# Kernel tuning notes

Hardware: AMD Instinct MI355X
Metric: run time of the kernel (lower is better)

The kernel has to match this reference:

```python
import jax, jax.numpy as jnp
import numpy as np
from jax.ops import segment_sum, segment_max

N, E, DS, DZ = 16384, 262144, 384, 128
H, D, PQ, PV = 12, 16, 4, 8
EPS = 1e-8


def _quat_to_rot(q):
    q = q / jnp.linalg.norm(q, axis=-1, keepdims=True)
    w, x, y, z = q[:, 0], q[:, 1], q[:, 2], q[:, 3]
    R = jnp.stack([
        1 - 2 * (y * y + z * z), 2 * (x * y - w * z), 2 * (x * z + w * y),
        2 * (x * y + w * z), 1 - 2 * (x * x + z * z), 2 * (y * z - w * x),
        2 * (x * z - w * y), 2 * (y * z + w * x), 1 - 2 * (x * x + y * y),
    ], axis=-1).reshape(-1, 3, 3)
    return R


def setup_inputs() -> dict:
    key = jax.random.key(0)
    ks = jax.random.split(key, 20)
    s = jax.random.normal(ks[0], (N, DS), jnp.float32)
    z = jax.random.normal(ks[1], (E, DZ), jnp.float32)
    edge_index = jax.random.randint(ks[2], (E, 2), 0, N, jnp.int64)
    # valid rigid frames: rotation from random unit quaternion + translation
    R = _quat_to_rot(jax.random.normal(ks[3], (N, 4), jnp.float32))
    t = jax.random.normal(ks[4], (N, 3), jnp.float32)
    f = jnp.zeros((N, 4, 4), jnp.float32).at[:, :3, :3].set(R)
    f = f.at[:, :3, 3].set(t).at[:, 3, 3].set(1.0)

    def lin(k, dout, din):
        return jax.random.normal(k, (dout, din), jnp.float32) / np.sqrt(din)

    hc, hpqk, hpv = H * D, H * PQ * 3, H * PV * 3
    s_out_dim = H * (D * 2 + PV * 4)
    params = dict(
        Wq=lin(ks[5], hc, DS), bq=jnp.zeros((hc,), jnp.float32),
        Wk=lin(ks[6], hc, DS), bk=jnp.zeros((hc,), jnp.float32),
        Wv=lin(ks[7], hc, DS), bv=jnp.zeros((hc,), jnp.float32),
        Wb=lin(ks[8], H, DZ), bb=jnp.zeros((H,), jnp.float32),
        Wqp=lin(ks[9], hpqk, DS), bqp=jnp.zeros((hpqk,), jnp.float32),
        Wkp=lin(ks[10], hpqk, DS), bkp=jnp.zeros((hpqk,), jnp.float32),
        Wvp=lin(ks[11], hpv, DS), bvp=jnp.zeros((hpv,), jnp.float32),
        head_weights=jnp.full((H,), 0.541324854612918, jnp.float32),
        Wpair=lin(ks[12], hc, DZ), bpair=jnp.zeros((hc,), jnp.float32),
        Wo=lin(ks[13], DS, s_out_dim), bo=jnp.zeros((DS,), jnp.float32),
    )
    return dict(s=s, z=z, f=f, edge_index=edge_index, **params)


def _ipa(s, z, f, edge_index, Wq, bq, Wk, bk, Wv, bv, Wb, bb,
         Wqp, bqp, Wkp, bkp, Wvp, bvp, head_weights, Wpair, bpair, Wo, bo):
    n = s.shape[0]
    R, t = f[:, :3, :3], f[:, :3, 3]
    idx_i, idx_j = edge_index[:, 0], edge_index[:, 1]

    norm_attn = (3.0 * D) ** 0.5          # (1/(3d))**-0.5 as in source
    norm_bias = 3.0 ** 0.5
    norm_pt = -0.5 * (3.0 * (PQ * 9.0 / 2)) ** 0.5

    q = (s @ Wq.T + bq).reshape(n, H, D)
    k = (s @ Wk.T + bk).reshape(n, H, D)
    v = (s @ Wv.T + bv).reshape(n, H, D)

    def to_global(pts):  # [n,H,P,3] local -> global
        return jnp.einsum('nij,nhpj->nhpi', R, pts) + t[:, None, None, :]

    q_pts = to_global((s @ Wqp.T + bqp).reshape(n, H, PQ, 3))
    k_pts = to_global((s @ Wkp.T + bkp).reshape(n, H, PQ, 3))
    v_pts = to_global((s @ Wvp.T + bvp).reshape(n, H, PV, 3))

    # scalar QK term + learned pair bias, per edge [E,H]
    attn = jnp.einsum('ehd,ehd->eh', q[idx_i], k[idx_j]) * norm_attn
    attn = attn + (z @ Wb.T + bb) * norm_bias
    # point-distance term
    diff = q_pts[idx_i] - k_pts[idx_j]            # [E,H,PQ,3]
    pt_att = (diff ** 2).sum((-1, -2))            # [E,H]
    pt_att = pt_att * (jax.nn.softplus(head_weights) * norm_pt)
    attn = attn + pt_att

    # segment softmax over edges grouped by destination node idx_i
    m = segment_max(attn, idx_i, num_segments=n)          # [N,H]
    ex = jnp.exp(attn - m[idx_i])
    denom = segment_sum(ex, idx_i, num_segments=n)
    a = ex / denom[idx_i]                                  # [E,H]

    o = segment_sum(a[:, :, None] * v[idx_j], idx_i, num_segments=n)  # [N,H,D]
    o = o.reshape(n, H * D)

    o_pts_g = segment_sum(a[:, :, None, None] * v_pts[idx_j], idx_i,
                          num_segments=n)                  # [N,H,PV,3]
    o_pts_g = o_pts_g.reshape(n, H * PV, 3)
    # invert_apply: R^T (p - t)
    o_pts = jnp.einsum('nji,npj->npi', R, o_pts_g - t[:, None, :])
    o_pts_norm = jnp.sqrt((o_pts ** 2).sum(-1) + EPS)      # [N,H*PV]
    o_pts_flat = o_pts.reshape(n, H * PV * 3)

    v_pair = (z @ Wpair.T + bpair).reshape(-1, H, D)       # [E,H,D]
    o_pair = segment_sum(a[:, :, None] * v_pair, idx_i, num_segments=n)
    o_pair = o_pair.reshape(n, H * D)

    o_s = jnp.concatenate([o, o_pts_flat, o_pts_norm, o_pair], axis=-1)
    return o_s @ Wo.T + bo


def reference(s, z, f, edge_index, Wq, bq, Wk, bk, Wv, bv, Wb, bb,
              Wqp, bqp, Wkp, bkp, Wvp, bvp, head_weights, Wpair, bpair, Wo, bo):
    s_out = _ipa(s, z, f, edge_index, Wq, bq, Wk, bk, Wv, bv, Wb, bb,
                 Wqp, bqp, Wkp, bkp, Wvp, bvp, head_weights, Wpair, bpair, Wo, bo)
    return (s_out, z)
```

## Files before the change

kernel.cpp:

```cpp
#include <hip/hip_runtime.h>

#define NNODE 16384
#define NEDGE 262144
#define DS    384
#define DZ    128
#define NH    12
#define HD    16
#define HC    192
#define HPQK  144
#define HPV   288
#define NCAT  1152
#define FEAT  2144
#define SOUT  384

typedef _Float16 f16;
typedef _Float16 f16x8 __attribute__((ext_vector_type(8)));
typedef _Float16 f16x4 __attribute__((ext_vector_type(4)));
typedef _Float16 f16x2 __attribute__((ext_vector_type(2)));
typedef float    f32x4v __attribute__((ext_vector_type(4)));

#define AS3(p) ((__attribute__((address_space(3))) void*)(p))
#define AS1(p) ((const __attribute__((address_space(1))) void*)(p))
#define WAVE_LDS_FENCE() asm volatile("s_waitcnt lgkmcnt(0)" ::: "memory")

__global__ void k_prep(const float* __restrict__ Wq, const float* __restrict__ Wk,
                       const float* __restrict__ Wv, const float* __restrict__ Wqp,
                       const float* __restrict__ Wkp, const float* __restrict__ Wvp,
                       const float* __restrict__ bq, const float* __restrict__ bk,
                       const float* __restrict__ bv, const float* __restrict__ bqp,
                       const float* __restrict__ bkp, const float* __restrict__ bvp,
                       const float* __restrict__ Wb, const float* __restrict__ Wo,
                       const float* __restrict__ Wpair, const float* __restrict__ bpair,
                       const float* __restrict__ hw,
                       f16* __restrict__ Wcat, float* __restrict__ bcat,
                       f16* __restrict__ Wb16, f16* __restrict__ M2,
                       float* __restrict__ gamv)
{
    int t = blockIdx.x * 256 + threadIdx.x;
    const int T0 = NCAT * DS;
    const int T1 = T0 + NCAT;
    const int T2 = T1 + 16 * DZ;
    const int T3 = T2 + SOUT * FEAT;
    const int T4 = T3 + NH;
    if (t < T0) {
        int r = t / DS, c = t - r * DS;
        float v;
        if      (r < 192) v = Wq [(r      ) * DS + c];
        else if (r < 384) v = Wk [(r - 192) * DS + c];
        else if (r < 576) v = Wv [(r - 384) * DS + c];
        else if (r < 720) v = Wqp[(r - 576) * DS + c];
        else if (r < 864) v = Wkp[(r - 720) * DS + c];
        else              v = Wvp[(r - 864) * DS + c];
        Wcat[t] = (f16)v;
    } else if (t < T1) {
        int r = t - T0;
        float v;
        if      (r < 192) v = bq [r];
        else if (r < 384) v = bk [r - 192];
        else if (r < 576) v = bv [r - 384];
        else if (r < 720) v = bqp[r - 576];
        else if (r < 864) v = bkp[r - 720];
        else              v = bvp[r - 864];
        bcat[r] = v;
    } else if (t < T2) {
        int q = t - T1;
        Wb16[q] = (q < NH * DZ) ? (f16)Wb[q] : (f16)0.0f;
    } else if (t < T3) {
        int q = t - T2;
        int r = q / FEAT, c = q - r * FEAT;
        float v = 0.f;
        if (c < 576) {
            v = Wo[r * 768 + c];
        } else if (c < 2112) {
            int h = (c - 576) >> 7, cc = (c - 576) & 127;
            float acc = 0.f;
            #pragma unroll
            for (int d = 0; d < 16; ++d)
                acc += Wo[r * 768 + 576 + h * 16 + d] * Wpair[(h * 16 + d) * DZ + cc];
            v = acc;
        } else if (c < 2124) {
            int h = c - 2112;
            float acc = 0.f;
            #pragma unroll
            for (int d = 0; d < 16; ++d)
                acc += Wo[r * 768 + 576 + h * 16 + d] * bpair[h * 16 + d];
            v = acc;
        }
        M2[q] = (f16)v;
    } else if (t < T4) {
        int h = t - T3;
        gamv[h] = -3.67423461f * log1pf(__expf(hw[h]));
    }
}

__global__ void k_convert_s(const float4* __restrict__ s4, f16* __restrict__ s16)
{
    int t = blockIdx.x * 256 + threadIdx.x;
    float4 v = s4[t];
    f16x4 o = { (f16)v.x, (f16)v.y, (f16)v.z, (f16)v.w };
    *(f16x4*)(s16 + 4 * (size_t)t) = o;
}

__global__ void k_convert_z(const float* __restrict__ z, const int* __restrict__ inv,
                            f16* __restrict__ z16s)
{
    int t = blockIdx.x * 256 + threadIdx.x;
    int e = t >> 1, half = t & 1;
    int pos = inv[e];
    const float4* zr = (const float4*)(z + (size_t)e * DZ + half * 64);
    f16* zo = z16s + (size_t)pos * DZ + half * 64;
    #pragma unroll
    for (int c = 0; c < 16; ++c) {
        float4 v = zr[c];
        f16x4 o = { (f16)v.x, (f16)v.y, (f16)v.z, (f16)v.w };
        *(f16x4*)(zo + 4 * c) = o;
    }
}

__global__ __launch_bounds__(256) void k_zbias(const f16* __restrict__ z16s,
                                               const f16* __restrict__ Wb16,
                                               const float* __restrict__ bb,
                                               float* __restrict__ zbias)
{
    const int wv = threadIdx.x >> 6, lane = threadIdx.x & 63;
    const int row0 = (blockIdx.x * 4 + wv) * 64;
    f16x8 bf[4];
    #pragma unroll
    for (int ks = 0; ks < 4; ++ks)
        bf[ks] = *(const f16x8*)(Wb16 + (lane & 15) * DZ + ks * 32 + (lane >> 4) * 8);
    #pragma unroll
    for (int tt = 0; tt < 4; ++tt) {
        int ra = row0 + tt * 16 + (lane & 15);
        f32x4v acc = {};
        #pragma unroll
        for (int ks = 0; ks < 4; ++ks) {
            f16x8 af = *(const f16x8*)(z16s + (size_t)ra * DZ + ks * 32 + (lane >> 4) * 8);
            acc = __builtin_amdgcn_mfma_f32_16x16x32_f16(af, bf[ks], acc, 0, 0, 0);
        }
        int col = lane & 15;
        if (col < NH) {
            #pragma unroll
            for (int r = 0; r < 4; ++r) {
                int row = row0 + tt * 16 + (lane >> 4) * 4 + r;
                zbias[(size_t)row * NH + col] = (acc[r] + bb[col]) * 1.73205081f;
            }
        }
    }
}

__global__ __launch_bounds__(256) void k_gemm(const f16* __restrict__ A, const f16* __restrict__ B,
                                              const float* __restrict__ bias, float* __restrict__ C,
                                              int M, int N, int K)
{
    __shared__ __align__(16) f16 As[128 * 32];
    __shared__ __align__(16) f16 Bs[128 * 32];
    const int tid = threadIdx.x;
    const int wave = tid >> 6, lane = tid & 63;
    const int bm = blockIdx.x, bn = blockIdx.y;
    const int wm = (wave >> 1) * 64, wn = (wave & 1) * 64;
    f32x4v acc[4][4] = {};
    const int srow = wave * 16 + (lane >> 2);
    const int scol = (lane & 3) * 8;
    const f16* gA0 = A + (size_t)(bm * 128 + srow) * K + scol;
    const f16* gA1 = A + (size_t)(bm * 128 + srow + 64) * K + scol;
    const f16* gB0 = B + (size_t)(bn * 128 + srow) * K + scol;
    const f16* gB1 = B + (size_t)(bn * 128 + srow + 64) * K + scol;
    f16* lA0 = As + wave * 512;
    f16* lA1 = As + (wave + 4) * 512;
    f16* lB0 = Bs + wave * 512;
    f16* lB1 = Bs + (wave + 4) * 512;
    const int fr = lane & 15, fc = (lane >> 4) * 8;
    const int nK = K >> 5;
    for (int kk = 0; kk < nK; ++kk) {
        __syncthreads();
        __builtin_amdgcn_global_load_lds(AS1(gA0), AS3(lA0), 16, 0, 0);
        __builtin_amdgcn_global_load_lds(AS1(gA1), AS3(lA1), 16, 0, 0);
        __builtin_amdgcn_global_load_lds(AS1(gB0), AS3(lB0), 16, 0, 0);
        __builtin_amdgcn_global_load_lds(AS1(gB1), AS3(lB1), 16, 0, 0);
        gA0 += 32; gA1 += 32; gB0 += 32; gB1 += 32;
        __syncthreads();
        f16x8 af[4], bf[4];
        #pragma unroll
        for (int mi = 0; mi < 4; ++mi)
            af[mi] = *(const f16x8*)(As + (wm + mi * 16 + fr) * 32 + fc);
        #pragma unroll
        for (int ni = 0; ni < 4; ++ni)
            bf[ni] = *(const f16x8*)(Bs + (wn + ni * 16 + fr) * 32 + fc);
        #pragma unroll
        for (int mi = 0; mi < 4; ++mi)
            #pragma unroll
            for (int ni = 0; ni < 4; ++ni)
                acc[mi][ni] = __builtin_amdgcn_mfma_f32_16x16x32_f16(af[mi], bf[ni], acc[mi][ni], 0, 0, 0);
    }
    const int r0 = bm * 128 + wm + (lane >> 4) * 4;
    const int c0 = bn * 128 + wn + (lane & 15);
    #pragma unroll
    for (int mi = 0; mi < 4; ++mi)
        #pragma unroll
        for (int ni = 0; ni < 4; ++ni) {
            int col = c0 + ni * 16;
            float b = bias[col];
            #pragma unroll
            for (int r = 0; r < 4; ++r) {
                int row = r0 + mi * 16 + r;
                C[(size_t)row * N + col] = acc[mi][ni][r] + b;
            }
        }
}

__global__ __launch_bounds__(64) void k_nodepost(const float* __restrict__ raw, const float* __restrict__ fmat,
        f16* __restrict__ Q16, f16* __restrict__ K16, f16* __restrict__ V16,
        f16* __restrict__ QP16, f16* __restrict__ KP16, f16* __restrict__ VP16)
{
    int n = blockIdx.x, l = threadIdx.x;
    const float* r = raw + (size_t)n * NCAT;
    #pragma unroll
    for (int q = 0; q < 3; ++q) {
        int c = q * 64 + l;
        Q16[(size_t)n * HC + c] = (f16)r[c];
        K16[(size_t)n * HC + c] = (f16)r[HC + c];
        V16[(size_t)n * HC + c] = (f16)r[2 * HC + c];
    }
    const float* fp = fmat + (size_t)n * 16;
    float R00 = fp[0], R01 = fp[1], R02 = fp[2],  t0 = fp[3];
    float R10 = fp[4], R11 = fp[5], R12 = fp[6],  t1 = fp[7];
    float R20 = fp[8], R21 = fp[9], R22 = fp[10], t2 = fp[11];
    if (l < 48) {
        const float* p = r + 576 + 3 * l;
        float x = p[0], y = p[1], zz = p[2];
        QP16[(size_t)n * HPQK + 3 * l + 0] = (f16)(R00 * x + R01 * y + R02 * zz + t0);
        QP16[(size_t)n * HPQK + 3 * l + 1] = (f16)(R10 * x + R11 * y + R12 * zz + t1);
        QP16[(size_t)n * HPQK + 3 * l + 2] = (f16)(R20 * x + R21 * y + R22 * zz + t2);
        const float* p2 = r + 720 + 3 * l;
        float x2 = p2[0], y2 = p2[1], z2 = p2[2];
        KP16[(size_t)n * HPQK + 3 * l + 0] = (f16)(R00 * x2 + R01 * y2 + R02 * z2 + t0);
        KP16[(size_t)n * HPQK + 3 * l + 1] = (f16)(R10 * x2 + R11 * y2 + R12 * z2 + t1);
        KP16[(size_t)n * HPQK + 3 * l + 2] = (f16)(R20 * x2 + R21 * y2 + R22 * z2 + t2);
    }
    {
        const float* p = r + 864 + 3 * l;
        float x = p[0], y = p[1], zz = p[2];
        VP16[(size_t)n * HPV + 3 * l + 0] = (f16)(R00 * x + R01 * y + R02 * zz + t0);
        VP16[(size_t)n * HPV + 3 * l + 1] = (f16)(R10 * x + R11 * y + R12 * zz + t1);
        VP16[(size_t)n * HPV + 3 * l + 2] = (f16)(R20 * x + R21 * y + R22 * zz + t2);
    }
    if (l < 32) {
        int tt = 64 + l;
        const float* p = r + 864 + 3 * tt;
        float x = p[0], y = p[1], zz = p[2];
        VP16[(size_t)n * HPV + 3 * tt + 0] = (f16)(R00 * x + R01 * y + R02 * zz + t0);
        VP16[(size_t)n * HPV + 3 * tt + 1] = (f16)(R10 * x + R11 * y + R12 * zz + t1);
        VP16[(size_t)n * HPV + 3 * tt + 2] = (f16)(R20 * x + R21 * y + R22 * zz + t2);
    }
}

__global__ void k_zero(int* counts, int* cursor) {
    int t = blockIdx.x * 256 + threadIdx.x;
    if (t < NNODE) counts[t] = 0;
    else if (t < 2 * NNODE) cursor[t - NNODE] = 0;
}
__global__ void k_count(const int* __restrict__ ei, int* counts) {
    int e = blockIdx.x * 256 + threadIdx.x;
    if (e < NEDGE) atomicAdd(&counts[ei[2 * e]], 1);
}
__global__ void k_scan(const int* __restrict__ counts, int* __restrict__ rowptr) {
    __shared__ int lds[256];
    int t = threadIdx.x;
    const int per = NNODE / 256;
    int s = 0;
    for (int i = 0; i < per; ++i) s += counts[t * per + i];
    lds[t] = s; __syncthreads();
    for (int off = 1; off < 256; off <<= 1) {
        int v = (t >= off) ? lds[t - off] : 0;
        __syncthreads();
        lds[t] += v;
        __syncthreads();
    }
    int run = (t == 0) ? 0 : lds[t - 1];
    for (int i = 0; i < per; ++i) { rowptr[t * per + i] = run; run += counts[t * per + i]; }
    if (t == 255) rowptr[NNODE] = run;
}
__global__ void k_scatter(const int* __restrict__ ei, const int* __restrict__ rowptr,
                          int* cursor, int* __restrict__ inv, int* __restrict__ jsorted) {
    int e = blockIdx.x * 256 + threadIdx.x;
    if (e < NEDGE) {
        int i = ei[2 * e];
        int pos = rowptr[i] + atomicAdd(&cursor[i], 1);
        inv[e] = pos;
        jsorted[pos] = ei[2 * e + 1];
    }
}

__global__ __launch_bounds__(256) void k_att(
    const int* __restrict__ rowptr, const int* __restrict__ jsorted,
    const float* __restrict__ zbias,
    const f16* __restrict__ Q16, const f16* __restrict__ K16,
    const f16* __restrict__ QP16, const f16* __restrict__ KP16,
    const float* __restrict__ gamv, f16* __restrict__ a16, f16* __restrict__ feat)
{
    __shared__ f16 qsh[4][HC];
    __shared__ f16 qpsh[4][HPQK];
    const int wv = threadIdx.x >> 6, lane = threadIdx.x & 63;
    const int n = blockIdx.x * 4 + wv;
    const int base = rowptr[n], deg = rowptr[n + 1] - base;
    for (int c = lane; c < HC; c += 64)   qsh[wv][c]  = Q16[(size_t)n * HC + c];
    for (int c = lane; c < HPQK; c += 64) qpsh[wv][c] = QP16[(size_t)n * HPQK + c];
    __syncthreads();

    float gam[NH];
    #pragma unroll
    for (int h = 0; h < NH; ++h) gam[h] = gamv[h];

    float lg[NH];
    #pragma unroll
    for (int h = 0; h < NH; ++h) lg[h] = -1e30f;

    auto compute_lg = [&](int off) {
        int pos = base + off + lane;
        int j = jsorted[pos];
        const float4* zbp = (const float4*)(zbias + (size_t)pos * NH);
        float4 zb0 = zbp[0], zb1 = zbp[1], zb2 = zbp[2];
        float zb[NH] = { zb0.x, zb0.y, zb0.z, zb0.w, zb1.x, zb1.y, zb1.z, zb1.w,
                         zb2.x, zb2.y, zb2.z, zb2.w };
        const f16x8* kr = (const f16x8*)(K16 + (size_t)j * HC);
        const f16* kpp = KP16 + (size_t)j * HPQK;
        #pragma unroll
        for (int h = 0; h < NH; ++h) {
            f16x8 k0 = kr[2 * h], k1 = kr[2 * h + 1];
            f16x8 q0 = *(const f16x8*)&qsh[wv][16 * h];
            f16x8 q1 = *(const f16x8*)&qsh[wv][16 * h + 8];
            float d = 0.f;
            #pragma unroll
            for (int u = 0; u < 8; ++u)
                d += (float)q0[u] * (float)k0[u] + (float)q1[u] * (float)k1[u];
            float pt = 0.f;
            #pragma unroll
            for (int c = 0; c < 3; ++c) {
                f16x4 kpc = *(const f16x4*)(kpp + 12 * h + 4 * c);
                f16x4 qpc = *(const f16x4*)&qpsh[wv][12 * h + 4 * c];
                #pragma unroll
                for (int u = 0; u < 4; ++u) {
                    float dd = (float)qpc[u] - (float)kpc[u];
                    pt += dd * dd;
                }
            }
            lg[h] = 6.92820323f * d + zb[h] + gam[h] * pt;
        }
    };

    if (lane < 32)
        feat[(size_t)n * FEAT + 2112 + lane] = (f16)((lane < NH && deg > 0) ? 1.0f : 0.0f);

    if (deg <= 64) {
        if (lane < deg) compute_lg(0);
        float il[NH];
        #pragma unroll
        for (int h = 0; h < NH; ++h) {
            float v = lg[h];
            for (int m2 = 1; m2 < 64; m2 <<= 1) v = fmaxf(v, __shfl_xor(v, m2));
            float e = __expf(lg[h] - v);
            float ssum = e;
            for (int m2 = 1; m2 < 64; m2 <<= 1) ssum += __shfl_xor(ssum, m2);
            lg[h] = e;
            il[h] = (ssum > 0.f) ? 1.0f / ssum : 0.f;
        }
        if (lane < deg) {
            f16x8 o0, o1;
            #pragma unroll
            for (int h = 0; h < 8; ++h) o0[h] = (f16)(lg[h] * il[h]);
            #pragma unroll
            for (int h = 8; h < 12; ++h) o1[h - 8] = (f16)(lg[h] * il[h]);
            o1[4] = o1[5] = o1[6] = o1[7] = (f16)0.0f;
            f16* ap = a16 + (size_t)(base + lane) * 16;
            *(f16x8*)ap = o0;
            *(f16x8*)(ap + 8) = o1;
        }
    } else {
        const int nch = (deg + 63) >> 6;
        float mx[NH];
        #pragma unroll
        for (int h = 0; h < NH; ++h) mx[h] = -1e30f;
        for (int c = 0; c < nch; ++c) {
            int cl = min(64, deg - c * 64);
            if (lane < cl) {
                compute_lg(c * 64);
                #pragma unroll
                for (int h = 0; h < NH; ++h) mx[h] = fmaxf(mx[h], lg[h]);
            }
        }
        #pragma unroll
        for (int h = 0; h < NH; ++h) {
            float v = mx[h];
            for (int m2 = 1; m2 < 64; m2 <<= 1) v = fmaxf(v, __shfl_xor(v, m2));
            mx[h] = v;
        }
        float ls[NH] = {};
        for (int c = 0; c < nch; ++c) {
            int cl = min(64, deg - c * 64);
            if (lane < cl) {
                compute_lg(c * 64);
                f16x8 o0, o1;
                #pragma unroll
                for (int h = 0; h < NH; ++h) {
                    float e = __expf(lg[h] - mx[h]);
                    ls[h] += e;
                    if (h < 8) o0[h] = (f16)e; else o1[h - 8] = (f16)e;
                }
                o1[4] = o1[5] = o1[6] = o1[7] = (f16)0.0f;
                f16* ap = a16 + (size_t)(base + c * 64 + lane) * 16;
                *(f16x8*)ap = o0;
                *(f16x8*)(ap + 8) = o1;
            }
        }
        float il[NH];
        #pragma unroll
        for (int h = 0; h < NH; ++h) {
            float v = ls[h];
            for (int m2 = 1; m2 < 64; m2 <<= 1) v += __shfl_xor(v, m2);
            il[h] = (v > 0.f) ? 1.0f / v : 0.f;
        }
        asm volatile("s_waitcnt vmcnt(0)" ::: "memory");
        for (int c = 0; c < nch; ++c) {
            int cl = min(64, deg - c * 64);
            if (lane < cl) {
                f16* ap = a16 + (size_t)(base + c * 64 + lane) * 16;
                f16x8 o0 = *(f16x8*)ap;
                f16x8 o1 = *(f16x8*)(ap + 8);
                #pragma unroll
                for (int h = 0; h < 8; ++h) o0[h] = (f16)((float)o0[h] * il[h]);
                #pragma unroll
                for (int h = 8; h < 12; ++h) o1[h - 8] = (f16)((float)o1[h - 8] * il[h]);
                *(f16x8*)ap = o0;
                *(f16x8*)(ap + 8) = o1;
            }
        }
    }
}

__global__ __launch_bounds__(256) void k_aggu(
    const int* __restrict__ rowptr, const f16* __restrict__ a16,
    const f16* __restrict__ z16s, f16* __restrict__ feat)
{
    __shared__ f16 ash[4][64 * 16];
    const int wv = threadIdx.x >> 6, lane = threadIdx.x & 63;
    const int n = blockIdx.x * 4 + wv;
    const int base = rowptr[n], deg = rowptr[n + 1] - base;
    float u0[NH] = {}, u1[NH] = {};
    const int nch = (deg + 63) >> 6;
    for (int c = 0; c < nch; ++c) {
        int cl = min(64, deg - c * 64);
        if (lane < cl) {
            const f16x8* ap = (const f16x8*)(a16 + (size_t)(base + c * 64 + lane) * 16);
            *(f16x8*)&ash[wv][lane * 16] = ap[0];
            *(f16x8*)&ash[wv][lane * 16 + 8] = ap[1];
        }
        WAVE_LDS_FENCE();
        for (int kk = 0; kk < cl; ++kk) {
            size_t pos = (size_t)(base + c * 64 + kk);
            f16x2 zv = *(const f16x2*)(z16s + pos * DZ + 2 * lane);
            float z0 = (float)zv[0], z1 = (float)zv[1];
            #pragma unroll
            for (int i = 0; i < 6; ++i) {
                f16x2 a2 = *(const f16x2*)&ash[wv][kk * 16 + 2 * i];
                float a0 = (float)a2[0], a1 = (float)a2[1];
                u0[2 * i]     += a0 * z0; u1[2 * i]     += a0 * z1;
                u0[2 * i + 1] += a1 * z0; u1[2 * i + 1] += a1 * z1;
            }
        }
        WAVE_LDS_FENCE();
    }
    f16* fo = feat + (size_t)n * FEAT + 576;
    #pragma unroll
    for (int h = 0; h < NH; ++h) {
        f16x2 o = { (f16)u0[h], (f16)u1[h] };
        *(f16x2*)(fo + h * DZ + 2 * lane) = o;
    }
}

__global__ __launch_bounds__(256) void k_aggv(
    const int* __restrict__ rowptr, const int* __restrict__ jsorted,
    const f16* __restrict__ a16, const f16* __restrict__ V16,
    const f16* __restrict__ VP16, const float* __restrict__ fmat,
    f16* __restrict__ feat)
{
    __shared__ f16 ash[4][64 * 16];
    __shared__ int jsh[4][64];
    __shared__ float psh[2][HPV];
    const int w4 = threadIdx.x >> 6;
    const int lane = threadIdx.x & 63;
    const int slot = w4 >> 1;
    const int role = w4 & 1;
    const int n = blockIdx.x * 2 + slot;
    const int base = rowptr[n], deg = rowptr[n + 1] - base;
    const int nch = (deg + 63) >> 6;

    float o0 = 0, o1 = 0, o2 = 0;
    const int hA = lane >> 4, hB = (64 + lane) >> 4, hC2 = (128 + lane) >> 4;
    float acc[5] = {};
    int hk[5];
    #pragma unroll
    for (int k = 0; k < 5; ++k) hk[k] = (k * 64 + lane) / 24;

    for (int c = 0; c < nch; ++c) {
        int cl = min(64, deg - c * 64);
        if (lane < cl) {
            size_t pos = (size_t)(base + c * 64 + lane);
            const f16x8* ap = (const f16x8*)(a16 + pos * 16);
            *(f16x8*)&ash[w4][lane * 16] = ap[0];
            *(f16x8*)&ash[w4][lane * 16 + 8] = ap[1];
            jsh[w4][lane] = jsorted[pos];
        }
        WAVE_LDS_FENCE();
        if (role == 0) {
            for (int kk = 0; kk < cl; ++kk) {
                int j = jsh[w4][kk];
                const f16* vr = V16 + (size_t)j * HC;
                float aA = (float)ash[w4][kk * 16 + hA];
                float aB = (float)ash[w4][kk * 16 + hB];
                float aC = (float)ash[w4][kk * 16 + hC2];
                o0 += aA * (float)vr[lane];
                o1 += aB * (float)vr[64 + lane];
                o2 += aC * (float)vr[128 + lane];
            }
        } else {
            for (int kk = 0; kk < cl; ++kk) {
                int j = jsh[w4][kk];
                const f16* vp = VP16 + (size_t)j * HPV;
                #pragma unroll
                for (int k = 0; k < 4; ++k)
                    acc[k] += (float)ash[w4][kk * 16 + hk[k]] * (float)vp[k * 64 + lane];
                if (lane < 32)
                    acc[4] += (float)ash[w4][kk * 16 + hk[4]] * (float)vp[256 + lane];
            }
        }
        WAVE_LDS_FENCE();
    }

    f16* fo = feat + (size_t)n * FEAT;
    if (role == 0) {
        fo[lane] = (f16)o0; fo[64 + lane] = (f16)o1; fo[128 + lane] = (f16)o2;
    } else {
        #pragma unroll
        for (int k = 0; k < 4; ++k) psh[slot][k * 64 + lane] = acc[k];
        if (lane < 32) psh[slot][256 + lane] = acc[4];
        WAVE_LDS_FENCE();
        const float* fp = fmat + (size_t)n * 16;
        float R00 = fp[0], R01 = fp[1], R02 = fp[2],  t0 = fp[3];
        float R10 = fp[4], R11 = fp[5], R12 = fp[6],  t1 = fp[7];
        float R20 = fp[8], R21 = fp[9], R22 = fp[10], t2 = fp[11];
        {
            int P = lane;
            float gx = psh[slot][3 * P] - t0, gy = psh[slot][3 * P + 1] - t1, gz = psh[slot][3 * P + 2] - t2;
            float lx = R00 * gx + R10 * gy + R20 * gz;
            float ly = R01 * gx + R11 * gy + R21 * gz;
            float lz = R02 * gx + R12 * gy + R22 * gz;
            fo[192 + 3 * P] = (f16)lx; fo[192 + 3 * P + 1] = (f16)ly; fo[192 + 3 * P + 2] = (f16)lz;
            fo[480 + P] = (f16)sqrtf(lx * lx + ly * ly + lz * lz + 1e-8f);
        }
        if (lane < 32) {
            int P = 64 + lane;
            float gx = psh[slot][3 * P] - t0, gy = psh[slot][3 * P + 1] - t1, gz = psh[slot][3 * P + 2] - t2;
            float lx = R00 * gx + R10 * gy + R20 * gz;
            float ly = R01 * gx + R11 * gy + R21 * gz;
            float lz = R02 * gx + R12 * gy + R22 * gz;
            fo[192 + 3 * P] = (f16)lx; fo[192 + 3 * P + 1] = (f16)ly; fo[192 + 3 * P + 2] = (f16)lz;
            fo[480 + P] = (f16)sqrtf(lx * lx + ly * ly + lz * lz + 1e-8f);
        }
    }
}

extern "C" void kernel_launch(void* const* d_in, const int* in_sizes, int n_in,
                              void* d_out, int out_size, void* d_ws, size_t ws_size,
                              hipStream_t stream)
{
    (void)in_sizes; (void)n_in; (void)out_size; (void)ws_size;
    const float* s     = (const float*)d_in[0];
    const float* z     = (const float*)d_in[1];
    const float* fmat  = (const float*)d_in[2];
    const int*   ei    = (const int*)d_in[3];
    const float* Wq    = (const float*)d_in[4];
    const float* bq    = (const float*)d_in[5];
    const float* Wk    = (const float*)d_in[6];
    const float* bk    = (const float*)d_in[7];
    const float* Wv    = (const float*)d_in[8];
    const float* bv    = (const float*)d_in[9];
    const float* Wb    = (const float*)d_in[10];
    const float* bb    = (const float*)d_in[11];
    const float* Wqp   = (const float*)d_in[12];
    const float* bqp   = (const float*)d_in[13];
    const float* Wkp   = (const float*)d_in[14];
    const float* bkp   = (const float*)d_in[15];
    const float* Wvp   = (const float*)d_in[16];
    const float* bvp   = (const float*)d_in[17];
    const float* hw    = (const float*)d_in[18];
    const float* Wpair = (const float*)d_in[19];
    const float* bpair = (const float*)d_in[20];
    const float* Wo    = (const float*)d_in[21];
    const float* bo    = (const float*)d_in[22];

    char* w = (char*)d_ws;
    auto alloc = [&](size_t bytes) { char* p = w; w += (bytes + 255) & ~(size_t)255; return p; };
    f16*   s16     = (f16*)  alloc((size_t)NNODE * DS * 2);
    f16*   Wcat    = (f16*)  alloc((size_t)NCAT * DS * 2);
    float* bcat    = (float*)alloc((size_t)NCAT * 4);
    f16*   Wb16    = (f16*)  alloc((size_t)16 * DZ * 2);
    f16*   M2      = (f16*)  alloc((size_t)SOUT * FEAT * 2);
    float* gamv    = (float*)alloc((size_t)NH * 4);
    int*   counts  = (int*)  alloc((size_t)NNODE * 4);
    int*   rowptr  = (int*)  alloc((size_t)(NNODE + 1) * 4);
    int*   cursor  = (int*)  alloc((size_t)NNODE * 4);
    int*   inv     = (int*)  alloc((size_t)NEDGE * 4);
    int*   jsorted = (int*)  alloc((size_t)NEDGE * 4);
    char*  U       = w;
    float* nodeRaw = (float*)U;
    f16*   feat    = (f16*)U;

    float* zout = (float*)d_out + (size_t)NNODE * DS;
    char*  zr   = (char*)zout;
    f16*   z16s  = (f16*)zr;   zr += (size_t)NEDGE * DZ * 2;
    float* zbias = (float*)zr; zr += (size_t)NEDGE * NH * 4;
    f16*   Q16   = (f16*)zr;   zr += (size_t)NNODE * HC * 2;
    f16*   K16   = (f16*)zr;   zr += (size_t)NNODE * HC * 2;
    f16*   QP16  = (f16*)zr;   zr += (size_t)NNODE * HPQK * 2;
    f16*   KP16  = (f16*)zr;   zr += (size_t)NNODE * HPQK * 2;
    f16*   V16   = (f16*)zr;   zr += (size_t)NNODE * HC * 2;
    f16*   VP16  = (f16*)zr;   zr += (size_t)NNODE * HPV * 2;
    f16*   a16   = (f16*)zr;

    const int PREP_T = NCAT * DS + NCAT + 16 * DZ + SOUT * FEAT + NH;
    k_prep<<<(PREP_T + 255) / 256, 256, 0, stream>>>(Wq, Wk, Wv, Wqp, Wkp, Wvp,
        bq, bk, bv, bqp, bkp, bvp, Wb, Wo, Wpair, bpair, hw, Wcat, bcat, Wb16, M2, gamv);
    k_zero<<<(2 * NNODE) / 256, 256, 0, stream>>>(counts, cursor);
    k_count<<<NEDGE / 256, 256, 0, stream>>>(ei, counts);
    k_scan<<<1, 256, 0, stream>>>(counts, rowptr);
    k_scatter<<<NEDGE / 256, 256, 0, stream>>>(ei, rowptr, cursor, inv, jsorted);
    k_convert_s<<<(NNODE * DS / 4) / 256, 256, 0, stream>>>((const float4*)s, s16);
    k_convert_z<<<(NEDGE * 2) / 256, 256, 0, stream>>>(z, inv, z16s);
    k_zbias<<<NEDGE / 256, 256, 0, stream>>>(z16s, Wb16, bb, zbias);
    k_gemm<<<dim3(NNODE / 128, NCAT / 128), 256, 0, stream>>>(s16, Wcat, bcat, nodeRaw,
        NNODE, NCAT, DS);
    k_nodepost<<<NNODE, 64, 0, stream>>>(nodeRaw, fmat, Q16, K16, V16, QP16, KP16, VP16);
    k_att<<<NNODE / 4, 256, 0, stream>>>(rowptr, jsorted, zbias, Q16, K16, QP16, KP16,
        gamv, a16, feat);
    k_aggu<<<NNODE / 4, 256, 0, stream>>>(rowptr, a16, z16s, feat);
    k_aggv<<<NNODE / 2, 256, 0, stream>>>(rowptr, jsorted, a16, V16, VP16, fmat, feat);
    hipMemcpyAsync(zout, z, (size_t)NEDGE * DZ * 4, hipMemcpyDeviceToDevice, stream);
    k_gemm<<<dim3(NNODE / 128, SOUT / 128), 256, 0, stream>>>(feat, M2, bo, (float*)d_out,
        NNODE, SOUT, FEAT);
}
```

Baseline: 434.7 us.

## Split attention into edge-parallel logits and 16-lane-per-node softmax; fp16 QKV GEMM output

The fused per-node attention kernel is replaced by two kernels. The first computes logits with one thread per sorted edge and writes them to an fp32 buffer. The second does the softmax with 16 lanes per node instead of a full 64-lane wave, which suits the average degree of 16. The node projection GEMM also writes fp16 output instead of fp32, halving that intermediate traffic. In exchange this adds an isorted array, an E×12 fp32 logits buffer that is written and read back, and one more kernel launch.

```diff
diff --git a/kernel.cpp b/kernel.cpp
--- a/kernel.cpp
+++ b/kernel.cpp
@@ -208,46 +208,106 @@
         }
 }
 
-__global__ __launch_bounds__(64) void k_nodepost(const float* __restrict__ raw, const float* __restrict__ fmat,
+__global__ __launch_bounds__(256) void k_gemm16(const f16* __restrict__ A, const f16* __restrict__ B,
+                                                const float* __restrict__ bias, f16* __restrict__ C,
+                                                int M, int N, int K)
+{
+    __shared__ __align__(16) f16 As[128 * 32];
+    __shared__ __align__(16) f16 Bs[128 * 32];
+    const int tid = threadIdx.x;
+    const int wave = tid >> 6, lane = tid & 63;
+    const int bm = blockIdx.x, bn = blockIdx.y;
+    const int wm = (wave >> 1) * 64, wn = (wave & 1) * 64;
+    f32x4v acc[4][4] = {};
+    const int srow = wave * 16 + (lane >> 2);
+    const int scol = (lane & 3) * 8;
+    const f16* gA0 = A + (size_t)(bm * 128 + srow) * K + scol;
+    const f16* gA1 = A + (size_t)(bm * 128 + srow + 64) * K + scol;
+    const f16* gB0 = B + (size_t)(bn * 128 + srow) * K + scol;
+    const f16* gB1 = B + (size_t)(bn * 128 + srow + 64) * K + scol;
+    f16* lA0 = As + wave * 512;
+    f16* lA1 = As + (wave + 4) * 512;
+    f16* lB0 = Bs + wave * 512;
+    f16* lB1 = Bs + (wave + 4) * 512;
+    const int fr = lane & 15, fc = (lane >> 4) * 8;
+    const int nK = K >> 5;
+    for (int kk = 0; kk < nK; ++kk) {
+        __syncthreads();
+        __builtin_amdgcn_global_load_lds(AS1(gA0), AS3(lA0), 16, 0, 0);
+        __builtin_amdgcn_global_load_lds(AS1(gA1), AS3(lA1), 16, 0, 0);
+        __builtin_amdgcn_global_load_lds(AS1(gB0), AS3(lB0), 16, 0, 0);
+        __builtin_amdgcn_global_load_lds(AS1(gB1), AS3(lB1), 16, 0, 0);
+        gA0 += 32; gA1 += 32; gB0 += 32; gB1 += 32;
+        __syncthreads();
+        f16x8 af[4], bf[4];
+        #pragma unroll
+        for (int mi = 0; mi < 4; ++mi)
+            af[mi] = *(const f16x8*)(As + (wm + mi * 16 + fr) * 32 + fc);
+        #pragma unroll
+        for (int ni = 0; ni < 4; ++ni)
+            bf[ni] = *(const f16x8*)(Bs + (wn + ni * 16 + fr) * 32 + fc);
+        #pragma unroll
+        for (int mi = 0; mi < 4; ++mi)
+            #pragma unroll
+            for (int ni = 0; ni < 4; ++ni)
+                acc[mi][ni] = __builtin_amdgcn_mfma_f32_16x16x32_f16(af[mi], bf[ni], acc[mi][ni], 0, 0, 0);
+    }
+    const int r0 = bm * 128 + wm + (lane >> 4) * 4;
+    const int c0 = bn * 128 + wn + (lane & 15);
+    #pragma unroll
+    for (int mi = 0; mi < 4; ++mi)
+        #pragma unroll
+        for (int ni = 0; ni < 4; ++ni) {
+            int col = c0 + ni * 16;
+            float b = bias[col];
+            #pragma unroll
+            for (int r = 0; r < 4; ++r) {
+                int row = r0 + mi * 16 + r;
+                C[(size_t)row * N + col] = (f16)(acc[mi][ni][r] + b);
+            }
+        }
+}
+
+__global__ __launch_bounds__(64) void k_nodepost(const f16* __restrict__ raw, const float* __restrict__ fmat,
         f16* __restrict__ Q16, f16* __restrict__ K16, f16* __restrict__ V16,
         f16* __restrict__ QP16, f16* __restrict__ KP16, f16* __restrict__ VP16)
 {
     int n = blockIdx.x, l = threadIdx.x;
-    const float* r = raw + (size_t)n * NCAT;
+    const f16* r = raw + (size_t)n * NCAT;
     #pragma unroll
     for (int q = 0; q < 3; ++q) {
         int c = q * 64 + l;
-        Q16[(size_t)n * HC + c] = (f16)r[c];
-        K16[(size_t)n * HC + c] = (f16)r[HC + c];
-        V16[(size_t)n * HC + c] = (f16)r[2 * HC + c];
+        Q16[(size_t)n * HC + c] = r[c];
+        K16[(size_t)n * HC + c] = r[HC + c];
+        V16[(size_t)n * HC + c] = r[2 * HC + c];
     }
     const float* fp = fmat + (size_t)n * 16;
     float R00 = fp[0], R01 = fp[1], R02 = fp[2],  t0 = fp[3];
     float R10 = fp[4], R11 = fp[5], R12 = fp[6],  t1 = fp[7];
     float R20 = fp[8], R21 = fp[9], R22 = fp[10], t2 = fp[11];
     if (l < 48) {
-        const float* p = r + 576 + 3 * l;
-        float x = p[0], y = p[1], zz = p[2];
+        const f16* p = r + 576 + 3 * l;
+        float x = (float)p[0], y = (float)p[1], zz = (float)p[2];
         QP16[(size_t)n * HPQK + 3 * l + 0] = (f16)(R00 * x + R01 * y + R02 * zz + t0);
         QP16[(size_t)n * HPQK + 3 * l + 1] = (f16)(R10 * x + R11 * y + R12 * zz + t1);
         QP16[(size_t)n * HPQK + 3 * l + 2] = (f16)(R20 * x + R21 * y + R22 * zz + t2);
-        const float* p2 = r + 720 + 3 * l;
-        float x2 = p2[0], y2 = p2[1], z2 = p2[2];
+        const f16* p2 = r + 720 + 3 * l;
+        float x2 = (float)p2[0], y2 = (float)p2[1], z2 = (float)p2[2];
         KP16[(size_t)n * HPQK + 3 * l + 0] = (f16)(R00 * x2 + R01 * y2 + R02 * z2 + t0);
         KP16[(size_t)n * HPQK + 3 * l + 1] = (f16)(R10 * x2 + R11 * y2 + R12 * z2 + t1);
         KP16[(size_t)n * HPQK + 3 * l + 2] = (f16)(R20 * x2 + R21 * y2 + R22 * z2 + t2);
     }
     {
-        const float* p = r + 864 + 3 * l;
-        float x = p[0], y = p[1], zz = p[2];
+        const f16* p = r + 864 + 3 * l;
+        float x = (float)p[0], y = (float)p[1], zz = (float)p[2];
         VP16[(size_t)n * HPV + 3 * l + 0] = (f16)(R00 * x + R01 * y + R02 * zz + t0);
         VP16[(size_t)n * HPV + 3 * l + 1] = (f16)(R10 * x + R11 * y + R12 * zz + t1);
         VP16[(size_t)n * HPV + 3 * l + 2] = (f16)(R20 * x + R21 * y + R22 * zz + t2);
     }
     if (l < 32) {
         int tt = 64 + l;
-        const float* p = r + 864 + 3 * tt;
-        float x = p[0], y = p[1], zz = p[2];
+        const f16* p = r + 864 + 3 * tt;
+        float x = (float)p[0], y = (float)p[1], zz = (float)p[2];
         VP16[(size_t)n * HPV + 3 * tt + 0] = (f16)(R00 * x + R01 * y + R02 * zz + t0);
         VP16[(size_t)n * HPV + 3 * tt + 1] = (f16)(R10 * x + R11 * y + R12 * zz + t1);
         VP16[(size_t)n * HPV + 3 * tt + 2] = (f16)(R20 * x + R21 * y + R22 * zz + t2);
@@ -281,133 +341,154 @@
     if (t == 255) rowptr[NNODE] = run;
 }
 __global__ void k_scatter(const int* __restrict__ ei, const int* __restrict__ rowptr,
-                          int* cursor, int* __restrict__ inv, int* __restrict__ jsorted) {
+                          int* cursor, int* __restrict__ inv, int* __restrict__ jsorted,
+                          int* __restrict__ isorted) {
     int e = blockIdx.x * 256 + threadIdx.x;
     if (e < NEDGE) {
         int i = ei[2 * e];
         int pos = rowptr[i] + atomicAdd(&cursor[i], 1);
         inv[e] = pos;
         jsorted[pos] = ei[2 * e + 1];
-    }
-}
-
-__global__ __launch_bounds__(256) void k_att(
-    const int* __restrict__ rowptr, const int* __restrict__ jsorted,
+        isorted[pos] = i;
+    }
+}
+
+__global__ __launch_bounds__(256) void k_logits2(
+    const int* __restrict__ isorted, const int* __restrict__ jsorted,
     const float* __restrict__ zbias,
     const f16* __restrict__ Q16, const f16* __restrict__ K16,
     const f16* __restrict__ QP16, const f16* __restrict__ KP16,
-    const float* __restrict__ gamv, f16* __restrict__ a16, f16* __restrict__ feat)
-{
-    __shared__ f16 qsh[4][HC];
-    __shared__ f16 qpsh[4][HPQK];
-    const int wv = threadIdx.x >> 6, lane = threadIdx.x & 63;
-    const int n = blockIdx.x * 4 + wv;
+    const float* __restrict__ gamv, float* __restrict__ attn)
+{
+    const int pos = blockIdx.x * 256 + threadIdx.x;
+    const int i = isorted[pos], j = jsorted[pos];
+    const f16x8* qr = (const f16x8*)(Q16 + (size_t)i * HC);
+    const f16x8* kr = (const f16x8*)(K16 + (size_t)j * HC);
+    const f16* qpp = QP16 + (size_t)i * HPQK;
+    const f16* kpp = KP16 + (size_t)j * HPQK;
+    const float4* zbp = (const float4*)(zbias + (size_t)pos * NH);
+    float4 zb0 = zbp[0], zb1 = zbp[1], zb2 = zbp[2];
+    float zb[NH] = { zb0.x, zb0.y, zb0.z, zb0.w, zb1.x, zb1.y, zb1.z, zb1.w,
+                     zb2.x, zb2.y, zb2.z, zb2.w };
+    float out[NH];
+    #pragma unroll
+    for (int h = 0; h < NH; ++h) {
+        f16x8 q0 = qr[2 * h], q1 = qr[2 * h + 1];
+        f16x8 k0 = kr[2 * h], k1 = kr[2 * h + 1];
+        float d = 0.f;
+        #pragma unroll
+        for (int u = 0; u < 8; ++u)
+            d += (float)q0[u] * (float)k0[u] + (float)q1[u] * (float)k1[u];
+        float pt = 0.f;
+        #pragma unroll
+        for (int c = 0; c < 3; ++c) {
+            f16x4 qpc = *(const f16x4*)(qpp + 12 * h + 4 * c);
+            f16x4 kpc = *(const f16x4*)(kpp + 12 * h + 4 * c);
+            #pragma unroll
+            for (int u = 0; u < 4; ++u) {
+                float dd = (float)qpc[u] - (float)kpc[u];
+                pt += dd * dd;
+            }
+        }
+        out[h] = 6.92820323f * d + zb[h] + gamv[h] * pt;
+    }
+    float4* ao = (float4*)(attn + (size_t)pos * NH);
+    ao[0] = make_float4(out[0], out[1], out[2], out[3]);
+    ao[1] = make_float4(out[4], out[5], out[6], out[7]);
+    ao[2] = make_float4(out[8], out[9], out[10], out[11]);
+}
+
+__global__ __launch_bounds__(256) void k_soft(
+    const int* __restrict__ rowptr, const float* __restrict__ attn,
+    f16* __restrict__ a16, f16* __restrict__ feat)
+{
+    const int lane = threadIdx.x & 63, wv = threadIdx.x >> 6;
+    const int slot = lane >> 4, el = lane & 15;
+    const int n = blockIdx.x * 16 + wv * 4 + slot;
     const int base = rowptr[n], deg = rowptr[n + 1] - base;
-    for (int c = lane; c < HC; c += 64)   qsh[wv][c]  = Q16[(size_t)n * HC + c];
-    for (int c = lane; c < HPQK; c += 64) qpsh[wv][c] = QP16[(size_t)n * HPQK + c];
-    __syncthreads();
-
-    float gam[NH];
-    #pragma unroll
-    for (int h = 0; h < NH; ++h) gam[h] = gamv[h];
+
+    f16* fo = feat + (size_t)n * FEAT;
+    fo[2112 + el]      = (f16)((el < NH && deg > 0) ? 1.0f : 0.0f);
+    fo[2112 + 16 + el] = (f16)0.0f;
 
     float lg[NH];
-    #pragma unroll
-    for (int h = 0; h < NH; ++h) lg[h] = -1e30f;
-
-    auto compute_lg = [&](int off) {
-        int pos = base + off + lane;
-        int j = jsorted[pos];
-        const float4* zbp = (const float4*)(zbias + (size_t)pos * NH);
-        float4 zb0 = zbp[0], zb1 = zbp[1], zb2 = zbp[2];
-        float zb[NH] = { zb0.x, zb0.y, zb0.z, zb0.w, zb1.x, zb1.y, zb1.z, zb1.w,
-                         zb2.x, zb2.y, zb2.z, zb2.w };
-        const f16x8* kr = (const f16x8*)(K16 + (size_t)j * HC);
-        const f16* kpp = KP16 + (size_t)j * HPQK;
-        #pragma unroll
-        for (int h = 0; h < NH; ++h) {
-            f16x8 k0 = kr[2 * h], k1 = kr[2 * h + 1];
-            f16x8 q0 = *(const f16x8*)&qsh[wv][16 * h];
-            f16x8 q1 = *(const f16x8*)&qsh[wv][16 * h + 8];
-            float d = 0.f;
-            #pragma unroll
-            for (int u = 0; u < 8; ++u)
-                d += (float)q0[u] * (float)k0[u] + (float)q1[u] * (float)k1[u];
-            float pt = 0.f;
-            #pragma unroll
-            for (int c = 0; c < 3; ++c) {
-                f16x4 kpc = *(const f16x4*)(kpp + 12 * h + 4 * c);
-                f16x4 qpc = *(const f16x4*)&qpsh[wv][12 * h + 4 * c];
-                #pragma unroll
-                for (int u = 0; u < 4; ++u) {
-                    float dd = (float)qpc[u] - (float)kpc[u];
-                    pt += dd * dd;
-                }
-            }
-            lg[h] = 6.92820323f * d + zb[h] + gam[h] * pt;
-        }
-    };
-
-    if (lane < 32)
-        feat[(size_t)n * FEAT + 2112 + lane] = (f16)((lane < NH && deg > 0) ? 1.0f : 0.0f);
-
-    if (deg <= 64) {
-        if (lane < deg) compute_lg(0);
-        float il[NH];
+    if (deg <= 16) {
+        if (el < deg) {
+            const float4* ar = (const float4*)(attn + (size_t)(base + el) * NH);
+            float4 a0 = ar[0], a1 = ar[1], a2 = ar[2];
+            lg[0]=a0.x; lg[1]=a0.y; lg[2]=a0.z; lg[3]=a0.w;
+            lg[4]=a1.x; lg[5]=a1.y; lg[6]=a1.z; lg[7]=a1.w;
+            lg[8]=a2.x; lg[9]=a2.y; lg[10]=a2.z; lg[11]=a2.w;
+        } else {
+            #pragma unroll
+            for (int h = 0; h < NH; ++h) lg[h] = -1e30f;
+        }
         #pragma unroll
         for (int h = 0; h < NH; ++h) {
             float v = lg[h];
-            for (int m2 = 1; m2 < 64; m2 <<= 1) v = fmaxf(v, __shfl_xor(v, m2));
+            v = fmaxf(v, __shfl_xor(v, 1));
+            v = fmaxf(v, __shfl_xor(v, 2));
+            v = fmaxf(v, __shfl_xor(v, 4));
+            v = fmaxf(v, __shfl_xor(v, 8));
             float e = __expf(lg[h] - v);
             float ssum = e;
-            for (int m2 = 1; m2 < 64; m2 <<= 1) ssum += __shfl_xor(ssum, m2);
-            lg[h] = e;
-            il[h] = (ssum > 0.f) ? 1.0f / ssum : 0.f;
-        }
-        if (lane < deg) {
+            ssum += __shfl_xor(ssum, 1);
+            ssum += __shfl_xor(ssum, 2);
+            ssum += __shfl_xor(ssum, 4);
+            ssum += __shfl_xor(ssum, 8);
+            lg[h] = (ssum > 0.f) ? e / ssum : 0.f;
+        }
+        if (el < deg) {
             f16x8 o0, o1;
             #pragma unroll
-            for (int h = 0; h < 8; ++h) o0[h] = (f16)(lg[h] * il[h]);
-            #pragma unroll
-            for (int h = 8; h < 12; ++h) o1[h - 8] = (f16)(lg[h] * il[h]);
+            for (int h = 0; h < 8; ++h) o0[h] = (f16)lg[h];
+            #pragma unroll
+            for (int h = 8; h < 12; ++h) o1[h - 8] = (f16)lg[h];
             o1[4] = o1[5] = o1[6] = o1[7] = (f16)0.0f;
-            f16* ap = a16 + (size_t)(base + lane) * 16;
+            f16* ap = a16 + (size_t)(base + el) * 16;
             *(f16x8*)ap = o0;
             *(f16x8*)(ap + 8) = o1;
         }
     } else {
-        const int nch = (deg + 63) >> 6;
+        const int nch = (deg + 15) >> 4;
         float mx[NH];
         #pragma unroll
         for (int h = 0; h < NH; ++h) mx[h] = -1e30f;
         for (int c = 0; c < nch; ++c) {
-            int cl = min(64, deg - c * 64);
-            if (lane < cl) {
-                compute_lg(c * 64);
+            int idx = c * 16 + el;
+            if (idx < deg) {
+                const float4* ar = (const float4*)(attn + (size_t)(base + idx) * NH);
+                float4 a0 = ar[0], a1 = ar[1], a2 = ar[2];
+                float v[NH] = { a0.x,a0.y,a0.z,a0.w, a1.x,a1.y,a1.z,a1.w, a2.x,a2.y,a2.z,a2.w };
                 #pragma unroll
-                for (int h = 0; h < NH; ++h) mx[h] = fmaxf(mx[h], lg[h]);
+                for (int h = 0; h < NH; ++h) mx[h] = fmaxf(mx[h], v[h]);
             }
         }
         #pragma unroll
         for (int h = 0; h < NH; ++h) {
             float v = mx[h];
-            for (int m2 = 1; m2 < 64; m2 <<= 1) v = fmaxf(v, __shfl_xor(v, m2));
+            v = fmaxf(v, __shfl_xor(v, 1));
+            v = fmaxf(v, __shfl_xor(v, 2));
+            v = fmaxf(v, __shfl_xor(v, 4));
+            v = fmaxf(v, __shfl_xor(v, 8));
             mx[h] = v;
         }
         float ls[NH] = {};
         for (int c = 0; c < nch; ++c) {
-            int cl = min(64, deg - c * 64);
-            if (lane < cl) {
-                compute_lg(c * 64);
+            int idx = c * 16 + el;
+            if (idx < deg) {
+                const float4* ar = (const float4*)(attn + (size_t)(base + idx) * NH);
+                float4 a0 = ar[0], a1 = ar[1], a2 = ar[2];
+                float v[NH] = { a0.x,a0.y,a0.z,a0.w, a1.x,a1.y,a1.z,a1.w, a2.x,a2.y,a2.z,a2.w };
                 f16x8 o0, o1;
                 #pragma unroll
                 for (int h = 0; h < NH; ++h) {
-                    float e = __expf(lg[h] - mx[h]);
+                    float e = __expf(v[h] - mx[h]);
                     ls[h] += e;
                     if (h < 8) o0[h] = (f16)e; else o1[h - 8] = (f16)e;
                 }
                 o1[4] = o1[5] = o1[6] = o1[7] = (f16)0.0f;
-                f16* ap = a16 + (size_t)(base + c * 64 + lane) * 16;
+                f16* ap = a16 + (size_t)(base + idx) * 16;
                 *(f16x8*)ap = o0;
                 *(f16x8*)(ap + 8) = o1;
             }
@@ -416,14 +497,16 @@
         #pragma unroll
         for (int h = 0; h < NH; ++h) {
             float v = ls[h];
-            for (int m2 = 1; m2 < 64; m2 <<= 1) v += __shfl_xor(v, m2);
+            v += __shfl_xor(v, 1);
+            v += __shfl_xor(v, 2);
+            v += __shfl_xor(v, 4);
+            v += __shfl_xor(v, 8);
             il[h] = (v > 0.f) ? 1.0f / v : 0.f;
         }
-        asm volatile("s_waitcnt vmcnt(0)" ::: "memory");
         for (int c = 0; c < nch; ++c) {
-            int cl = min(64, deg - c * 64);
-            if (lane < cl) {
-                f16* ap = a16 + (size_t)(base + c * 64 + lane) * 16;
+            int idx = c * 16 + el;
+            if (idx < deg) {
+                f16* ap = a16 + (size_t)(base + idx) * 16;
                 f16x8 o0 = *(f16x8*)ap;
                 f16x8 o1 = *(f16x8*)(ap + 8);
                 #pragma unroll
@@ -611,8 +694,10 @@
     int*   cursor  = (int*)  alloc((size_t)NNODE * 4);
     int*   inv     = (int*)  alloc((size_t)NEDGE * 4);
     int*   jsorted = (int*)  alloc((size_t)NEDGE * 4);
+    int*   isorted = (int*)  alloc((size_t)NEDGE * 4);
+    float* attn    = (float*)alloc((size_t)NEDGE * NH * 4);
     char*  U       = w;
-    float* nodeRaw = (float*)U;
+    f16*   raw16   = (f16*)U;
     f16*   feat    = (f16*)U;
 
     float* zout = (float*)d_out + (size_t)NNODE * DS;
@@ -633,15 +718,16 @@
     k_zero<<<(2 * NNODE) / 256, 256, 0, stream>>>(counts, cursor);
     k_count<<<NEDGE / 256, 256, 0, stream>>>(ei, counts);
     k_scan<<<1, 256, 0, stream>>>(counts, rowptr);
-    k_scatter<<<NEDGE / 256, 256, 0, stream>>>(ei, rowptr, cursor, inv, jsorted);
+    k_scatter<<<NEDGE / 256, 256, 0, stream>>>(ei, rowptr, cursor, inv, jsorted, isorted);
     k_convert_s<<<(NNODE * DS / 4) / 256, 256, 0, stream>>>((const float4*)s, s16);
     k_convert_z<<<(NEDGE * 2) / 256, 256, 0, stream>>>(z, inv, z16s);
     k_zbias<<<NEDGE / 256, 256, 0, stream>>>(z16s, Wb16, bb, zbias);
-    k_gemm<<<dim3(NNODE / 128, NCAT / 128), 256, 0, stream>>>(s16, Wcat, bcat, nodeRaw,
+    k_gemm16<<<dim3(NNODE / 128, NCAT / 128), 256, 0, stream>>>(s16, Wcat, bcat, raw16,
         NNODE, NCAT, DS);
-    k_nodepost<<<NNODE, 64, 0, stream>>>(nodeRaw, fmat, Q16, K16, V16, QP16, KP16, VP16);
-    k_att<<<NNODE / 4, 256, 0, stream>>>(rowptr, jsorted, zbias, Q16, K16, QP16, KP16,
-        gamv, a16, feat);
+    k_nodepost<<<NNODE, 64, 0, stream>>>(raw16, fmat, Q16, K16, V16, QP16, KP16, VP16);
+    k_logits2<<<NEDGE / 256, 256, 0, stream>>>(isorted, jsorted, zbias, Q16, K16,
+        QP16, KP16, gamv, attn);
+    k_soft<<<NNODE / 16, 256, 0, stream>>>(rowptr, attn, a16, feat);
     k_aggu<<<NNODE / 4, 256, 0, stream>>>(rowptr, a16, z16s, feat);
     k_aggv<<<NNODE / 2, 256, 0, stream>>>(rowptr, jsorted, a16, V16, VP16, fmat, feat);
     hipMemcpyAsync(zout, z, (size_t)NEDGE * DZ * 4, hipMemcpyDeviceToDevice, stream);
```

After: 431.4 us. Within noise of the previous version (-0.8%).
